# Optimization experiments

Hardware: AMD Instinct MI355X
Metric: run time of the kernel (lower is better)

The kernel has to match this reference:

```python
import jax, jax.numpy as jnp
import numpy as np

N, M, D, P = 4096, 8192, 512, 4
TEMP = 0.1  # SimCLR temperature


def setup_inputs() -> dict:
    key = jax.random.key(0)
    k1, k2, k3, k4 = jax.random.split(key, 4)
    queries = jax.random.normal(k1, (N, D), dtype=jnp.float32)
    keys = jax.random.normal(k2, (M, D), dtype=jnp.float32)
    # positives in lower half, ignores in upper half -> disjoint, no all--inf rows
    positive_indices = jax.random.randint(k3, (N, P), 0, M // 2)
    ignore_indices = jax.random.randint(k4, (N, P), M // 2, M)
    return dict(queries=queries, keys=keys,
                positive_indices=positive_indices, ignore_indices=ignore_indices)


def reference(queries, keys, positive_indices, ignore_indices):
    n, m = queries.shape[0], keys.shape[0]
    # score_fn = dot-product similarity, divided by temperature -> [N, M]
    scores = jnp.matmul(queries, keys.T) / TEMP
    rows = jnp.arange(n)[:, None]
    # scatter per-row index lists into boolean masks (duplicates collapse, as in torch)
    pos_mask = jnp.zeros((n, m), dtype=bool).at[rows, positive_indices].set(True)
    ign_mask = jnp.zeros((n, m), dtype=bool).at[rows, ignore_indices].set(True)
    neg_inf = jnp.array(-jnp.inf, dtype=scores.dtype)
    scores_m = jnp.where(ign_mask, neg_inf, scores)  # masked_fill(ignore, -inf)
    # scatter_logsumexp over positives == row-wise logsumexp restricted to pos_mask
    pos_lse = jax.nn.logsumexp(jnp.where(pos_mask, scores_m, neg_inf), axis=1)
    logp = pos_lse - jax.nn.logsumexp(scores_m, axis=1)
    loss = -jnp.sum(logp)
    preds = jnp.argmax(scores_m, axis=1)  # [N]
    corrects = jnp.any(positive_indices == preds[:, None], axis=1)  # [N] bool
    return (loss, corrects)
```

## Files before the change

kernel.cpp:

```cpp
#include <hip/hip_runtime.h>
#include <math.h>

#define N_Q 4096
#define M_K 8192
#define D_DIM 512
#define P_IDX 4
#define INV_TEMP 10.0f

#define NCHUNK 256

typedef __attribute__((ext_vector_type(8))) _Float16 f16x8;
typedef __attribute__((ext_vector_type(16))) float f32x16;

__global__ __launch_bounds__(256)
void pack_f16(const float* __restrict__ Q, const float* __restrict__ K,
              _Float16* __restrict__ Pq, _Float16* __restrict__ Pk,
              int qunits, int totunits)
{
    const int wunit = blockIdx.x * 4 + (threadIdx.x >> 6);
    if (wunit >= totunits) return;
    const bool isq = (wunit < qunits);
    const int u = isq ? wunit : wunit - qunits;
    const float* X = isq ? Q : K;
    _Float16* P = isq ? Pq : Pk;
    const float scale = isq ? INV_TEMP : 1.0f;
    const int rb = u >> 5, ks = u & 31;
    const int lane = threadIdx.x & 63;
    const int hi = lane >> 5, lx = lane & 31;
    const int row = rb * 32 + lx;
    const float4* src = (const float4*)(X + (size_t)row * D_DIM + ks * 16 + hi * 8);
    float4 v0 = src[0], v1 = src[1];
    f16x8 o;
    o[0] = (_Float16)(v0.x * scale); o[1] = (_Float16)(v0.y * scale);
    o[2] = (_Float16)(v0.z * scale); o[3] = (_Float16)(v0.w * scale);
    o[4] = (_Float16)(v1.x * scale); o[5] = (_Float16)(v1.y * scale);
    o[6] = (_Float16)(v1.z * scale); o[7] = (_Float16)(v1.w * scale);
    ((f16x8*)P)[(size_t)u * 64 + lane] = o;
}

#define MFMA_QUARTET(A0, A1, B0, B1)                                            \
    __builtin_amdgcn_s_setprio(1);                                              \
    acc[0][0] = __builtin_amdgcn_mfma_f32_32x32x16_f16(A0, B0, acc[0][0], 0, 0, 0); \
    acc[0][1] = __builtin_amdgcn_mfma_f32_32x32x16_f16(A0, B1, acc[0][1], 0, 0, 0); \
    acc[1][0] = __builtin_amdgcn_mfma_f32_32x32x16_f16(A1, B0, acc[1][0], 0, 0, 0); \
    acc[1][1] = __builtin_amdgcn_mfma_f32_32x32x16_f16(A1, B1, acc[1][1], 0, 0, 0); \
    __builtin_amdgcn_s_setprio(0);

__global__ __launch_bounds__(256)
void scores_mfma(const _Float16* __restrict__ Qp, const _Float16* __restrict__ Kp,
                 const int* __restrict__ ign, float4* __restrict__ part)
{
    const int tid = threadIdx.x;
    const int lane = tid & 63;
    const int wave = tid >> 6;
    const int wr = wave >> 1, wc = wave & 1;
    const int hi = lane >> 5, lx = lane & 31;
    const int bx = blockIdx.x;
    const int by = blockIdx.y;

    const f16x8* Kp8 = (const f16x8*)Kp;
    const f16x8* Qp8 = (const f16x8*)Qp;
    const f16x8* A0p = Kp8 + ((size_t)(bx * 4 + wr * 2 + 0) * 32) * 64 + lane;
    const f16x8* A1p = Kp8 + ((size_t)(bx * 4 + wr * 2 + 1) * 32) * 64 + lane;
    const f16x8* B0p = Qp8 + ((size_t)(by * 4 + wc * 2 + 0) * 32) * 64 + lane;
    const f16x8* B1p = Qp8 + ((size_t)(by * 4 + wc * 2 + 1) * 32) * 64 + lane;

    f32x16 acc[2][2];
#pragma unroll
    for (int i = 0; i < 2; ++i)
#pragma unroll
        for (int j = 0; j < 2; ++j) acc[i][j] = (f32x16)0.f;

    f16x8 rA0 = A0p[0],   rA1 = A1p[0],   rB0 = B0p[0],   rB1 = B1p[0];
    f16x8 sA0 = A0p[64],  sA1 = A1p[64],  sB0 = B0p[64],  sB1 = B1p[64];
    f16x8 tA0 = A0p[128], tA1 = A1p[128], tB0 = B0p[128], tB1 = B1p[128];
    f16x8 uA0 = A0p[192], uA1 = A1p[192], uB0 = B0p[192], uB1 = B1p[192];

    for (int ks = 0; ks < 32; ks += 4) {
        MFMA_QUARTET(rA0, rA1, rB0, rB1)
        if (ks + 4 < 32) {
            const int o = (ks + 4) * 64;
            rA0 = A0p[o]; rA1 = A1p[o]; rB0 = B0p[o]; rB1 = B1p[o];
        }
        MFMA_QUARTET(sA0, sA1, sB0, sB1)
        if (ks + 5 < 32) {
            const int o = (ks + 5) * 64;
            sA0 = A0p[o]; sA1 = A1p[o]; sB0 = B0p[o]; sB1 = B1p[o];
        }
        MFMA_QUARTET(tA0, tA1, tB0, tB1)
        if (ks + 6 < 32) {
            const int o = (ks + 6) * 64;
            tA0 = A0p[o]; tA1 = A1p[o]; tB0 = B0p[o]; tB1 = B1p[o];
        }
        MFMA_QUARTET(uA0, uA1, uB0, uB1)
        if (ks + 7 < 32) {
            const int o = (ks + 7) * 64;
            uA0 = A0p[o]; uA1 = A1p[o]; uB0 = B0p[o]; uB1 = B1p[o];
        }
    }

    const int kbase = bx * 128 + wr * 64 + 4 * hi;
    const int chunk = bx * 4 + wr * 2 + hi;
#pragma unroll
    for (int j = 0; j < 2; ++j) {
        const int qrow = by * 128 + wc * 64 + j * 32 + lx;
        const int4 ig = ((const int4*)ign)[qrow];
        float bm = -INFINITY; int bi = 0x7fffffff;
#pragma unroll
        for (int i = 0; i < 2; ++i) {
#pragma unroll
            for (int r = 0; r < 16; ++r) {
                const int col = kbase + i * 32 + (r & 3) + 8 * (r >> 2);
                float x = acc[i][j][r];
                if (col == ig.x || col == ig.y || col == ig.z || col == ig.w)
                    x = -INFINITY;
                acc[i][j][r] = x;
                if (x > bm || (x == bm && col < bi)) { bm = x; bi = col; }
            }
        }
        float se = 0.f;
#pragma unroll
        for (int i = 0; i < 2; ++i)
#pragma unroll
            for (int r = 0; r < 16; ++r)
                se += __expf(acc[i][j][r] - bm);
        part[(size_t)qrow * NCHUNK + chunk] =
            make_float4(bm, se, __int_as_float(bi), 0.f);
    }
}

__global__ __launch_bounds__(256)
void combine_kernel(const float4* __restrict__ part,
                    const float* __restrict__ Q, const float* __restrict__ K,
                    const int* __restrict__ pos,
                    float* __restrict__ logp, float* __restrict__ corrects)
{
    const int row = blockIdx.x * 4 + (threadIdx.x >> 6);
    const int lane = threadIdx.x & 63;

    float4 p0 = part[(size_t)row * NCHUNK + lane];
    float m = p0.x, s = p0.y, av = p0.x;
    int ai = __float_as_int(p0.z);
#pragma unroll
    for (int k = 1; k < 4; ++k) {
        float4 p = part[(size_t)row * NCHUNK + k * 64 + lane];
        int oi = __float_as_int(p.z);
        float nm = fmaxf(m, p.x);
        s = s * expf(m - nm) + p.y * expf(p.x - nm);
        m = nm;
        if (p.x > av || (p.x == av && oi < ai)) { av = p.x; ai = oi; }
    }

#pragma unroll
    for (int off = 32; off >= 1; off >>= 1) {
        float om = __shfl_xor(m, off);
        float os = __shfl_xor(s, off);
        float oav = __shfl_xor(av, off);
        int oi = __shfl_xor(ai, off);
        float nm = fmaxf(m, om);
        s = s * expf(m - nm) + os * expf(om - nm);
        m = nm;
        if (oav > av || (oav == av && oi < ai)) { av = oav; ai = oi; }
    }
    float lse = m + logf(s);

    int pi[4];
#pragma unroll
    for (int p = 0; p < 4; ++p) pi[p] = pos[row * P_IDX + p];

    const float4* q4 = (const float4*)(Q + (size_t)row * D_DIM);
    float4 qa = q4[lane * 2], qb = q4[lane * 2 + 1];
    float d[4];
#pragma unroll
    for (int p = 0; p < 4; ++p) {
        const float4* k4 = (const float4*)(K + (size_t)pi[p] * D_DIM);
        float4 ka = k4[lane * 2], kb = k4[lane * 2 + 1];
        d[p] = qa.x * ka.x + qa.y * ka.y + qa.z * ka.z + qa.w * ka.w
             + qb.x * kb.x + qb.y * kb.y + qb.z * kb.z + qb.w * kb.w;
    }
#pragma unroll
    for (int off = 32; off >= 1; off >>= 1) {
#pragma unroll
        for (int p = 0; p < 4; ++p) d[p] += __shfl_xor(d[p], off);
    }

    if (lane == 0) {
        float ps[4];
#pragma unroll
        for (int p = 0; p < 4; ++p) ps[p] = d[p] * INV_TEMP;
        const bool v1 = (pi[1] != pi[0]);
        const bool v2 = (pi[2] != pi[0]) && (pi[2] != pi[1]);
        const bool v3 = (pi[3] != pi[0]) && (pi[3] != pi[1]) && (pi[3] != pi[2]);
        float pm = ps[0];
        if (v1) pm = fmaxf(pm, ps[1]);
        if (v2) pm = fmaxf(pm, ps[2]);
        if (v3) pm = fmaxf(pm, ps[3]);
        float pse = expf(ps[0] - pm);
        if (v1) pse += expf(ps[1] - pm);
        if (v2) pse += expf(ps[2] - pm);
        if (v3) pse += expf(ps[3] - pm);
        float pos_lse = pm + logf(pse);
        logp[row] = pos_lse - lse;
        bool corr = (ai == pi[0]) || (ai == pi[1]) || (ai == pi[2]) || (ai == pi[3]);
        corrects[row] = corr ? 1.0f : 0.0f;
    }
}

__global__ __launch_bounds__(256)
void loss_kernel(const float* __restrict__ logp, float* __restrict__ out)
{
    __shared__ float sm[256];
    const int t = threadIdx.x;
    float s = 0.f;
    for (int i = t; i < N_Q; i += 256) s += logp[i];
    sm[t] = s;
    __syncthreads();
    for (int off = 128; off >= 1; off >>= 1) {
        if (t < off) sm[t] += sm[t + off];
        __syncthreads();
    }
    if (t == 0) out[0] = -sm[0];
}

extern "C" void kernel_launch(void* const* d_in, const int* in_sizes, int n_in,
                              void* d_out, int out_size, void* d_ws, size_t ws_size,
                              hipStream_t stream)
{
    const float* Q = (const float*)d_in[0];
    const float* K = (const float*)d_in[1];
    const int* pos = (const int*)d_in[2];
    const int* ign = (const int*)d_in[3];
    float* out = (float*)d_out;

    _Float16* Qp = (_Float16*)d_ws;
    _Float16* Kp = Qp + (size_t)N_Q * D_DIM;
    float4* part = (float4*)(Kp + (size_t)M_K * D_DIM);
    float* logp = (float*)(part + (size_t)N_Q * NCHUNK);

    const int qunits = N_Q / 32 * 32;
    const int totunits = qunits + M_K / 32 * 32;
    pack_f16<<<totunits / 4, 256, 0, stream>>>(Q, K, Qp, Kp, qunits, totunits);

    dim3 gridA(M_K / 128, N_Q / 128);
    scores_mfma<<<gridA, 256, 0, stream>>>(Qp, Kp, ign, part);
    combine_kernel<<<N_Q / 4, 256, 0, stream>>>(part, Q, K, pos, logp, out + 1);
    loss_kernel<<<1, 256, 0, stream>>>(logp, out);
}
```

Measured before the change: 75.38 us.

## Widen score blocks to 8 waves with barrier-synced lockstep loads

The scores kernel now uses 512-thread blocks covering 256 keys by 128 queries, so eight waves share each query tile. The register prefetch depth drops from four stages to two. An s_barrier after each MFMA group keeps the waves in lockstep, which is meant to raise cache reuse of the shared operand loads. The cost is less latency hiding per wave and barrier stalls, while the grid shrinks to half as many larger blocks.

```diff
diff --git a/kernel.cpp b/kernel.cpp
--- a/kernel.cpp
+++ b/kernel.cpp
@@ -46,24 +46,25 @@
     acc[1][1] = __builtin_amdgcn_mfma_f32_32x32x16_f16(A1, B1, acc[1][1], 0, 0, 0); \
     __builtin_amdgcn_s_setprio(0);
 
-__global__ __launch_bounds__(256)
+__global__ __launch_bounds__(512)
 void scores_mfma(const _Float16* __restrict__ Qp, const _Float16* __restrict__ Kp,
                  const int* __restrict__ ign, float4* __restrict__ part)
 {
     const int tid = threadIdx.x;
     const int lane = tid & 63;
     const int wave = tid >> 6;
-    const int wr = wave >> 1, wc = wave & 1;
+    const int wr = wave >> 1;
+    const int wc = wave & 1;
     const int hi = lane >> 5, lx = lane & 31;
     const int bx = blockIdx.x;
     const int by = blockIdx.y;
 
     const f16x8* Kp8 = (const f16x8*)Kp;
     const f16x8* Qp8 = (const f16x8*)Qp;
-    const f16x8* A0p = Kp8 + ((size_t)(bx * 4 + wr * 2 + 0) * 32) * 64 + lane;
-    const f16x8* A1p = Kp8 + ((size_t)(bx * 4 + wr * 2 + 1) * 32) * 64 + lane;
-    const f16x8* B0p = Qp8 + ((size_t)(by * 4 + wc * 2 + 0) * 32) * 64 + lane;
-    const f16x8* B1p = Qp8 + ((size_t)(by * 4 + wc * 2 + 1) * 32) * 64 + lane;
+    const f16x8* A0p = Kp8 + ((size_t)((bx * 8 + wr * 2 + 0) * 32)) * 64 + lane;
+    const f16x8* A1p = Kp8 + ((size_t)((bx * 8 + wr * 2 + 1) * 32)) * 64 + lane;
+    const f16x8* B0p = Qp8 + ((size_t)((by * 4 + wc * 2 + 0) * 32)) * 64 + lane;
+    const f16x8* B1p = Qp8 + ((size_t)((by * 4 + wc * 2 + 1) * 32)) * 64 + lane;
 
     f32x16 acc[2][2];
 #pragma unroll
@@ -71,36 +72,26 @@
 #pragma unroll
         for (int j = 0; j < 2; ++j) acc[i][j] = (f32x16)0.f;
 
-    f16x8 rA0 = A0p[0],   rA1 = A1p[0],   rB0 = B0p[0],   rB1 = B1p[0];
-    f16x8 sA0 = A0p[64],  sA1 = A1p[64],  sB0 = B0p[64],  sB1 = B1p[64];
-    f16x8 tA0 = A0p[128], tA1 = A1p[128], tB0 = B0p[128], tB1 = B1p[128];
-    f16x8 uA0 = A0p[192], uA1 = A1p[192], uB0 = B0p[192], uB1 = B1p[192];
-
-    for (int ks = 0; ks < 32; ks += 4) {
-        MFMA_QUARTET(rA0, rA1, rB0, rB1)
-        if (ks + 4 < 32) {
-            const int o = (ks + 4) * 64;
-            rA0 = A0p[o]; rA1 = A1p[o]; rB0 = B0p[o]; rB1 = B1p[o];
+    f16x8 pA0 = A0p[0],  pA1 = A1p[0],  pB0 = B0p[0],  pB1 = B1p[0];
+    f16x8 sA0 = A0p[64], sA1 = A1p[64], sB0 = B0p[64], sB1 = B1p[64];
+
+    for (int ks = 0; ks < 32; ks += 2) {
+        MFMA_QUARTET(pA0, pA1, pB0, pB1)
+        asm volatile("s_barrier" ::: "memory");
+        if (ks + 2 < 32) {
+            const int o = (ks + 2) * 64;
+            pA0 = A0p[o]; pA1 = A1p[o]; pB0 = B0p[o]; pB1 = B1p[o];
         }
         MFMA_QUARTET(sA0, sA1, sB0, sB1)
-        if (ks + 5 < 32) {
-            const int o = (ks + 5) * 64;
+        asm volatile("s_barrier" ::: "memory");
+        if (ks + 3 < 32) {
+            const int o = (ks + 3) * 64;
             sA0 = A0p[o]; sA1 = A1p[o]; sB0 = B0p[o]; sB1 = B1p[o];
         }
-        MFMA_QUARTET(tA0, tA1, tB0, tB1)
-        if (ks + 6 < 32) {
-            const int o = (ks + 6) * 64;
-            tA0 = A0p[o]; tA1 = A1p[o]; tB0 = B0p[o]; tB1 = B1p[o];
-        }
-        MFMA_QUARTET(uA0, uA1, uB0, uB1)
-        if (ks + 7 < 32) {
-            const int o = (ks + 7) * 64;
-            uA0 = A0p[o]; uA1 = A1p[o]; uB0 = B0p[o]; uB1 = B1p[o];
-        }
-    }
-
-    const int kbase = bx * 128 + wr * 64 + 4 * hi;
-    const int chunk = bx * 4 + wr * 2 + hi;
+    }
+
+    const int kbase = bx * 256 + wr * 64 + 4 * hi;
+    const int chunk = bx * 8 + wr * 2 + hi;
 #pragma unroll
     for (int j = 0; j < 2; ++j) {
         const int qrow = by * 128 + wc * 64 + j * 32 + lx;
@@ -241,8 +232,8 @@
     const int totunits = qunits + M_K / 32 * 32;
     pack_f16<<<totunits / 4, 256, 0, stream>>>(Q, K, Qp, Kp, qunits, totunits);
 
-    dim3 gridA(M_K / 128, N_Q / 128);
-    scores_mfma<<<gridA, 256, 0, stream>>>(Qp, Kp, ign, part);
+    dim3 gridA(M_K / 256, N_Q / 128);
+    scores_mfma<<<gridA, 512, 0, stream>>>(Qp, Kp, ign, part);
     combine_kernel<<<N_Q / 4, 256, 0, stream>>>(part, Q, K, pos, logp, out + 1);
     loss_kernel<<<1, 256, 0, stream>>>(logp, out);
 }
```

New measurement: 79.42 us. +5.4%, slower.
